# Kernel optimization log

Measured on AMD Instinct MI355X. Metric: run time of the kernel, lower is better.

The kernel has to match this reference:

```python
import jax, jax.numpy as jnp
import numpy as np

COMMITMENT_COST = 0.25
DECAY = 0.99
EPSILON = 1e-05


def setup_inputs() -> dict:
    key = jax.random.key(0)
    k1, k2, k3, k4 = jax.random.split(key, 4)
    S, B, D, K = 256, 64, 512, 4096
    return {
        "inputs": jax.random.normal(k1, (S, B, D), dtype=jnp.float32),
        "embedding_weight": jax.random.normal(k2, (K, D), dtype=jnp.float32),
        "ema_w": jax.random.normal(k3, (K, D), dtype=jnp.float32),
        "ema_cluster_size": jax.random.uniform(k4, (K,), dtype=jnp.float32),
    }


def reference(inputs, embedding_weight, ema_w, ema_cluster_size):
    S, B, D = inputs.shape
    K = embedding_weight.shape[0]
    flat = inputs.reshape(-1, D)  # [N, D], N = S*B

    distances = (
        jnp.sum(flat * flat, axis=1, keepdims=True)
        + jnp.sum(embedding_weight * embedding_weight, axis=1)
        - 2.0 * flat @ embedding_weight.T
    )
    encoding_indices = jnp.argmin(distances, axis=1)  # [N]
    encodings = jax.nn.one_hot(encoding_indices, K, dtype=inputs.dtype)  # [N, K]

    # gather codebook rows (equivalent to encodings @ weight)
    quantized = jnp.take(embedding_weight, encoding_indices, axis=0).reshape(S, B, D)
    encodings_flat = encodings.reshape(S, B, K)

    # EMA codebook update (training-mode buffers; computed with stop_gradient semantics)
    counts = jnp.sum(encodings, axis=0)  # [K]
    new_cluster_size = ema_cluster_size * DECAY + (1.0 - DECAY) * counts
    n = jnp.sum(new_cluster_size)
    new_cluster_size = (new_cluster_size + EPSILON) / (n + K * EPSILON) * n
    dw = jax.ops.segment_sum(flat, encoding_indices, num_segments=K)  # encodings.T @ flat
    new_ema_w = ema_w * DECAY + (1.0 - DECAY) * dw
    new_embedding_weight = new_ema_w / new_cluster_size[:, None]

    # commitment loss (quantized detached)
    e_latent_loss = jnp.mean((jax.lax.stop_gradient(quantized) - inputs) ** 2)
    loss = COMMITMENT_COST * e_latent_loss

    # straight-through estimator
    quantized_st = inputs + jax.lax.stop_gradient(quantized - inputs)

    return (
        loss,
        quantized_st,
        encodings_flat,
        encoding_indices[:, None],
        new_embedding_weight,
        new_cluster_size,
        new_ema_w,
    )
```

## Files before the change

### kernel.cpp

```cpp
#include <hip/hip_runtime.h>
#include <hip/hip_bf16.h>
#include <cstdint>
#include <cstddef>

typedef __attribute__((ext_vector_type(8))) short short8;
typedef __attribute__((ext_vector_type(4))) float f32x4;

#define D_DIM 512
#define K_DIM 4096
#define N_ROWS 16384

#define DECAY_F 0.99f
#define OMD_F 0.01f
#define EPS_F 1e-5f
#define COMMIT_F 0.25f
#define MARGIN_F 0.75f

#define OFF_LOSS 0
#define OFF_QST 1
#define OFF_ENC (1 + 8388608)
#define OFF_IDX (OFF_ENC + 67108864)
#define OFF_NEW_W (OFF_IDX + 16384)
#define OFF_NEW_CS (OFF_NEW_W + 2097152)
#define OFF_NEW_EMA (OFF_NEW_CS + 4096)

#define WS_MINKEY 0
#define WS_COUNTS 131072
#define WS_E2 147456
#define WS_LOSSP 163840
#define WS_RCNT 164096
#define WS_OFFS 164112
#define WS_CURS 180496
#define WS_ROWL 196880
#define WS_ARENA 262416

#define AR_M1K 0
#define AR_M2V 4194304
#define AR_XHI 6291456
#define AR_EHI 23068672
#define AR_RROW 27262976
#define AR_RCUT 27328512
#define AR_NEED 27394048
#define WS_NEED (WS_ARENA + AR_NEED)

#define SCR0 8388612

__device__ __forceinline__ unsigned long long mkkey(float d, int c) {
  unsigned u = __float_as_uint(d);
  u ^= (unsigned)(((int)u) >> 31) | 0x80000000u;
  return ((unsigned long long)u << 32) | (unsigned)c;
}
__device__ __forceinline__ float keyval(unsigned long long k) {
  unsigned u = (unsigned)(k >> 32);
  u = (u & 0x80000000u) ? (u ^ 0x80000000u) : ~u;
  return __uint_as_float(u);
}
__device__ __forceinline__ void merge2(unsigned long long& k1, float& v2,
                                       unsigned long long ko, float v2o) {
  float v1 = keyval(k1), v1o = keyval(ko);
  float vmax = fmaxf(v1, v1o);
  v2 = fminf(fminf(v2, v2o), vmax);
  if (ko < k1) k1 = ko;
}
__device__ __forceinline__ unsigned pk2o(float a, float b) {
  unsigned ua = (__float_as_uint(a) + 0x8000u) & 0xFFFF0000u;
  unsigned ub = (__float_as_uint(b) + 0x8000u) & 0xFFFF0000u;
  return (ua >> 16) | ub;
}
__device__ __forceinline__ void gl_lds16(const void* g, void* l) {
  __builtin_amdgcn_global_load_lds(
      (const __attribute__((address_space(1))) unsigned int*)g,
      (__attribute__((address_space(3))) unsigned int*)l, 16, 0, 0);
}

__global__ void k_e2(const float* __restrict__ E, float* __restrict__ e2,
                     uint4* __restrict__ ehi, int* __restrict__ counts,
                     float* __restrict__ loss_part, int* __restrict__ rcnt) {
  int tid = threadIdx.x;
  int lane = tid & 63;
  int w = tid >> 6;
  int k = blockIdx.x * 4 + w;
  if (tid < 4) counts[blockIdx.x * 4 + tid] = 0;
  if (blockIdx.x == 0 && tid < 64) loss_part[tid] = 0.f;
  if (blockIdx.x == 1 && tid == 0) *rcnt = 0;
  const float4* ev = (const float4*)(E + (size_t)k * D_DIM);
  float4 a = ev[lane * 2], b = ev[lane * 2 + 1];
  uint4 h;
  h.x = pk2o(a.x, a.y);
  h.y = pk2o(a.z, a.w);
  h.z = pk2o(b.x, b.y);
  h.w = pk2o(b.z, b.w);
  ehi[(size_t)k * 64 + lane] = h;
  float s = a.x * a.x + a.y * a.y + a.z * a.z + a.w * a.w +
            b.x * b.x + b.y * b.y + b.z * b.z + b.w * b.w;
#pragma unroll
  for (int off = 32; off > 0; off >>= 1) s += __shfl_down(s, off, 64);
  if (lane == 0) e2[k] = s;
}

__global__ void k_conv(const float* __restrict__ src, uint4* __restrict__ hi) {
  int t = blockIdx.x * 256 + threadIdx.x;
  const float4* s4 = (const float4*)src;
  float4 a = s4[t * 2], b = s4[t * 2 + 1];
  uint4 h;
  h.x = pk2o(a.x, a.y);
  h.y = pk2o(a.z, a.w);
  h.z = pk2o(b.x, b.y);
  h.w = pk2o(b.z, b.w);
  hi[t] = h;
}

__global__ void k_scale_emaw(const float* __restrict__ ema_w, float* __restrict__ out) {
  int i = blockIdx.x * 256 + threadIdx.x;
  out[OFF_NEW_EMA + i] = DECAY_F * ema_w[i];
}

__global__ __launch_bounds__(256, 2) void k_gemm(
    const char* __restrict__ xhi, const char* __restrict__ ehi,
    const float* __restrict__ e2, unsigned long long* __restrict__ m1k,
    float* __restrict__ m2v, float* outp, int doZero) {
  extern __shared__ char smem[];
  const int tid = threadIdx.x;
  const int w = tid >> 6, lane = tid & 63;
  const int wr = w >> 1, wc = w & 1;
  const int l15 = lane & 15, g = lane >> 4;
  const int row0 = blockIdx.x * 128;
  const int col0 = blockIdx.y * 128;

  const char* srcBase = (w < 2) ? xhi : ehi;
  const int srcRow0 = (w < 2) ? (row0 + 64 * w) : (col0 + 64 * (w - 2));
  const int lr = lane >> 3;
  const int lc = lane & 7;
  const char* srcLane = srcBase + (size_t)(srcRow0 + lr) * 1024 + ((lc ^ lr) << 4);
  const int dstOff = w * 8192;

#define STAGE(c, b)                                       \
  {                                                       \
    const char* sp_ = srcLane + (c) * 128;                \
    char* lb_ = smem + (b) * 32768 + dstOff;              \
    _Pragma("unroll") for (int q = 0; q < 8; ++q)         \
        gl_lds16(sp_ + q * 8192, lb_ + q * 1024);         \
  }

  f32x4 acc[4][4];
  const f32x4 z = {0.f, 0.f, 0.f, 0.f};
#pragma unroll
  for (int i = 0; i < 4; ++i)
#pragma unroll
    for (int j = 0; j < 4; ++j) acc[i][j] = z;

  STAGE(0, 0);
  const int s0 = (g ^ (l15 & 7)) << 4;
  const int aRow = (wr * 64 + l15) * 128;
  const int bRow = (wc * 64 + l15) * 128;

  for (int c = 0; c < 8; ++c) {
    __syncthreads();
    if (c < 7) STAGE(c + 1, (c + 1) & 1);
    const char* Ab = smem + (c & 1) * 32768;
    const char* Bb = Ab + 16384;
    short8 a[2][4], b[2][4];
#pragma unroll
    for (int kk = 0; kk < 2; ++kk) {
      const int sw = s0 ^ (kk << 6);
#pragma unroll
      for (int i = 0; i < 4; ++i) {
        a[kk][i] = *(const short8*)(Ab + aRow + i * 2048 + sw);
        b[kk][i] = *(const short8*)(Bb + bRow + i * 2048 + sw);
      }
    }
#pragma unroll
    for (int kk = 0; kk < 2; ++kk)
#pragma unroll
      for (int i = 0; i < 4; ++i)
#pragma unroll
        for (int j = 0; j < 4; ++j)
          acc[i][j] = __builtin_amdgcn_mfma_f32_16x16x32_bf16(a[kk][i], b[kk][j], acc[i][j], 0, 0, 0);
  }
#undef STAGE

  __syncthreads();
  unsigned long long* lk = (unsigned long long*)smem;
  float* lv = (float*)(smem + 2048);
  float e2v[4];
#pragma unroll
  for (int j = 0; j < 4; ++j) e2v[j] = e2[col0 + wc * 64 + j * 16 + l15];

#pragma unroll
  for (int i = 0; i < 4; ++i) {
    int rowl = wr * 64 + i * 16 + (g << 2);
#pragma unroll
    for (int r = 0; r < 4; ++r) {
      unsigned long long k1 = 0;
      float v2 = 3.4e38f;
#pragma unroll
      for (int j = 0; j < 4; ++j) {
        float dv = fmaf(-2.f, acc[i][j][r], e2v[j]);
        unsigned long long kk = mkkey(dv, col0 + wc * 64 + j * 16 + l15);
        if (j == 0) k1 = kk;
        else merge2(k1, v2, kk, 3.4e38f);
      }
#pragma unroll
      for (int m = 1; m <= 8; m <<= 1) {
        unsigned long long ko = __shfl_xor(k1, m, 64);
        float vo = __shfl_xor(v2, m, 64);
        merge2(k1, v2, ko, vo);
      }
      if (l15 == 0) {
        lk[(rowl + r) * 2 + wc] = k1;
        lv[(rowl + r) * 2 + wc] = v2;
      }
    }
  }
  __syncthreads();
  if (tid < 128) {
    unsigned long long k1 = lk[tid * 2];
    float v2 = lv[tid * 2];
    merge2(k1, v2, lk[tid * 2 + 1], lv[tid * 2 + 1]);
    size_t o = (size_t)(row0 + tid) * 32 + blockIdx.y;
    m1k[o] = k1;
    m2v[o] = v2;
  }

  if (doZero) {
    const f32x4 z4 = {0.f, 0.f, 0.f, 0.f};
    float* encm1 = outp + (size_t)OFF_ENC - 1 + (size_t)row0 * K_DIM + col0;
#pragma unroll
    for (int q = 0; q < 16; ++q) {
      int s = tid + 256 * q;
      int r = s >> 5, c4 = s & 31;
      float* p = encm1 + (size_t)r * K_DIM + c4 * 4;
      if (row0 == 0 && col0 == 0 && s == 0) {
        outp[OFF_ENC + 0] = 0.f;
        outp[OFF_ENC + 1] = 0.f;
        outp[OFF_ENC + 2] = 0.f;
      } else {
        __builtin_nontemporal_store(z4, (f32x4*)p);
      }
    }
  }
}

__global__ void k_reduce(const unsigned long long* __restrict__ m1k,
                         const float* __restrict__ m2v,
                         unsigned long long* __restrict__ minkey,
                         int* __restrict__ rcnt, int* __restrict__ rrows,
                         float* __restrict__ rcut) {
  int row = blockIdx.x * 256 + threadIdx.x;
  const unsigned long long* kp = m1k + (size_t)row * 32;
  const float* vp = m2v + (size_t)row * 32;
  unsigned long long k1 = kp[0];
  float v2 = vp[0];
#pragma unroll 4
  for (int t = 1; t < 32; ++t) merge2(k1, v2, kp[t], vp[t]);
  float v1 = keyval(k1);
  if (v2 - v1 < MARGIN_F) {
    minkey[row] = ~0ull;
    int p = atomicAdd(rcnt, 1);
    rrows[p] = row;
    rcut[p] = v1 + MARGIN_F;
  } else {
    minkey[row] = k1;
  }
}

__global__ __launch_bounds__(256) void k_rescue(
    const float* __restrict__ flat, const float* __restrict__ E,
    const float* __restrict__ e2, const int* __restrict__ rcnt,
    const int* __restrict__ rrows, const float* __restrict__ rcut,
    const unsigned long long* __restrict__ m1k,
    unsigned long long* __restrict__ minkey) {
  __shared__ float sx[512];
  __shared__ unsigned long long skey[16];
  const int tid = threadIdx.x;
  const int sl = tid & 15;
  int cnt = *rcnt;
  if (cnt > N_ROWS) cnt = N_ROWS;
  for (int j = (int)blockIdx.x; j < cnt; j += (int)gridDim.x) {
    const int row = rrows[j];
    const float cutoff = rcut[j];
    __syncthreads();
    if (tid < 128) ((float4*)sx)[tid] = ((const float4*)(flat + (size_t)row * 512))[tid];
    __syncthreads();
    unsigned long long best = ~0ull;
    for (int b = 0; b < 32; ++b) {
      if (keyval(m1k[(size_t)row * 32 + b]) >= cutoff) continue;
      const int c0 = b * 128 + (tid >> 4);
#pragma unroll 2
      for (int p = 0; p < 8; ++p) {
        const int c = c0 + p * 16;
        const float4* ev = (const float4*)(E + (size_t)c * 512) + sl * 8;
        const float4* xv = (const float4*)sx + sl * 8;
        float s = 0.f;
#pragma unroll
        for (int q = 0; q < 8; ++q) {
          float4 e4 = ev[q];
          float4 x4 = xv[q];
          s = fmaf(e4.x, x4.x, s);
          s = fmaf(e4.y, x4.y, s);
          s = fmaf(e4.z, x4.z, s);
          s = fmaf(e4.w, x4.w, s);
        }
#pragma unroll
        for (int m = 1; m <= 8; m <<= 1) s += __shfl_xor(s, m, 64);
        if (sl == 0) {
          unsigned long long k = mkkey(fmaf(-2.f, s, e2[c]), c);
          if (k < best) best = k;
        }
      }
    }
    if (sl == 0) skey[tid >> 4] = best;
    __syncthreads();
    if (tid == 0) {
      unsigned long long m = skey[0];
#pragma unroll
      for (int t = 1; t < 16; ++t)
        if (skey[t] < m) m = skey[t];
      atomicMin(&minkey[row], m);
    }
  }
}

__global__ void k_zero(float* __restrict__ out) {
  const f32x4 z = {0.f, 0.f, 0.f, 0.f};
  f32x4* out4 = (f32x4*)(out + 8388612);
#pragma unroll
  for (int t = 0; t < 4; ++t) {
    int i = blockIdx.x * 1024 + t * 256 + threadIdx.x;
    if (i < 16777215) __builtin_nontemporal_store(z, out4 + i);
  }
  if (blockIdx.x == 0 && threadIdx.x == 0) {
    out[8388609] = 0.f;
    out[8388610] = 0.f;
    out[8388611] = 0.f;
    out[75497472] = 0.f;
  }
}

__global__ __launch_bounds__(1024) void k_prefix(const unsigned long long* __restrict__ minkey,
                                                 int* __restrict__ counts,
                                                 int* __restrict__ offs,
                                                 int* __restrict__ cursor) {
  __shared__ int lc[4096];
  __shared__ int wsum[16];
  const int tid = threadIdx.x;
  const int lane = tid & 63, w = tid >> 6;
#pragma unroll
  for (int t = 0; t < 4; ++t) lc[tid * 4 + t] = 0;
  __syncthreads();
#pragma unroll
  for (int t = 0; t < 16; ++t) {
    int c = (int)(unsigned)(minkey[tid + 1024 * t] & 0xffffffffull);
    atomicAdd(&lc[c], 1);
  }
  __syncthreads();
  int v[4];
  int loc = 0;
#pragma unroll
  for (int t = 0; t < 4; ++t) {
    v[t] = lc[tid * 4 + t];
    loc += v[t];
  }
  int scan = loc;
#pragma unroll
  for (int off = 1; off <= 32; off <<= 1) {
    int o = __shfl_up(scan, off, 64);
    if (lane >= off) scan += o;
  }
  if (lane == 63) wsum[w] = scan;
  __syncthreads();
  int base = 0;
  for (int i = 0; i < w; ++i) base += wsum[i];
  int run = base + scan - loc;
#pragma unroll
  for (int t = 0; t < 4; ++t) {
    counts[tid * 4 + t] = v[t];
    offs[tid * 4 + t] = run;
    cursor[tid * 4 + t] = run;
    run += v[t];
  }
}

__global__ void k_scatter(const unsigned long long* __restrict__ minkey,
                          int* __restrict__ cursor, int* __restrict__ rowl) {
  int n = blockIdx.x * 256 + threadIdx.x;
  int c = (int)(unsigned)(minkey[n] & 0xffffffffull);
  int pos = atomicAdd(&cursor[c], 1);
  rowl[pos] = n;
}

__global__ __launch_bounds__(256) void k_qdw(const float* __restrict__ flat,
                                             const float* __restrict__ E,
                                             const float* __restrict__ ema_w,
                                             const int* __restrict__ counts,
                                             const int* __restrict__ offs,
                                             const int* __restrict__ rowl,
                                             float* __restrict__ out,
                                             float* __restrict__ loss_part) {
  const int k = blockIdx.x;
  const int tid = threadIdx.x;
  const int cnt = counts[k];
  const int off = offs[k];
  const int d0 = tid * 2;
  const float ex = E[(size_t)k * D_DIM + d0];
  const float ey = E[(size_t)k * D_DIM + d0 + 1];
  float s0 = 0.f, s1 = 0.f, lsum = 0.f;
  for (int i = 0; i < cnt; ++i) {
    int r = rowl[off + i];
    const float* xr = flat + (size_t)r * D_DIM + d0;
    float xx = xr[0], xy = xr[1];
    size_t qb = (size_t)OFF_QST + (size_t)r * D_DIM + d0;
    out[qb] = xx + (ex - xx);
    out[qb + 1] = xy + (ey - xy);
    float dx = ex - xx, dy = ey - xy;
    lsum += dx * dx + dy * dy;
    s0 += xx;
    s1 += xy;
  }
  float e0 = DECAY_F * ema_w[(size_t)k * D_DIM + d0] + OMD_F * s0;
  float e1 = DECAY_F * ema_w[(size_t)k * D_DIM + d0 + 1] + OMD_F * s1;
  float cs = out[OFF_NEW_CS + k];
  size_t b = (size_t)k * D_DIM + d0;
  out[OFF_NEW_EMA + b] = e0;
  out[OFF_NEW_EMA + b + 1] = e1;
  out[OFF_NEW_W + b] = e0 / cs;
  out[OFF_NEW_W + b + 1] = e1 / cs;
#pragma unroll
  for (int o = 32; o > 0; o >>= 1) lsum += __shfl_down(lsum, o, 64);
  __shared__ float ws4[4];
  if ((tid & 63) == 0) ws4[tid >> 6] = lsum;
  __syncthreads();
  if (tid == 0 && cnt > 0)
    atomicAdd(&loss_part[k & 63], ws4[0] + ws4[1] + ws4[2] + ws4[3]);
}

__global__ void k_quant(const float* __restrict__ flat, const float* __restrict__ E,
                        const unsigned long long* __restrict__ minkey,
                        float* __restrict__ out, float* emaw,
                        float* __restrict__ loss_part) {
  int tid = threadIdx.x;
  int lane = tid & 63;
  int rw = tid >> 6;
  int n = blockIdx.x * 4 + rw;
  int idx = (int)(unsigned)(minkey[n] & 0xffffffffull);
  const float4* xv = (const float4*)(flat + (size_t)n * D_DIM);
  const float4* ev = (const float4*)(E + (size_t)idx * D_DIM);
  float* emarow = emaw + (size_t)idx * D_DIM;
  float s = 0.f;
#pragma unroll
  for (int t = 0; t < 2; ++t) {
    int p = lane + 64 * t;
    float4 x = xv[p];
    float4 e = ev[p];
    size_t qb = (size_t)OFF_QST + (size_t)n * D_DIM + (size_t)p * 4;
    out[qb + 0] = x.x + (e.x - x.x);
    out[qb + 1] = x.y + (e.y - x.y);
    out[qb + 2] = x.z + (e.z - x.z);
    out[qb + 3] = x.w + (e.w - x.w);
    float dx = e.x - x.x, dy = e.y - x.y, dz = e.z - x.z, dw = e.w - x.w;
    s += dx * dx + dy * dy + dz * dz + dw * dw;
    atomicAdd(emarow + p * 4 + 0, OMD_F * x.x);
    atomicAdd(emarow + p * 4 + 1, OMD_F * x.y);
    atomicAdd(emarow + p * 4 + 2, OMD_F * x.z);
    atomicAdd(emarow + p * 4 + 3, OMD_F * x.w);
  }
#pragma unroll
  for (int off = 32; off > 0; off >>= 1) s += __shfl_down(s, off, 64);
  __shared__ float ws4[4];
  if (lane == 0) ws4[rw] = s;
  __syncthreads();
  if (tid == 0) atomicAdd(&loss_part[blockIdx.x & 63], ws4[0] + ws4[1] + ws4[2] + ws4[3]);
}

__global__ void k_decode(const unsigned long long* __restrict__ minkey,
                         int* __restrict__ counts,
                         const float* __restrict__ loss_part,
                         float* __restrict__ out, int withCounts, int withLoss) {
  int n = blockIdx.x * 256 + threadIdx.x;
  int c = (int)(unsigned)(minkey[n] & 0xffffffffull);
  out[OFF_IDX + n] = (float)c;
  if (withCounts) atomicAdd(&counts[c], 1);
  if (n == N_ROWS - 1) out[(size_t)OFF_ENC + (size_t)n * K_DIM + 4095] = 0.f;
  out[(size_t)OFF_ENC + (size_t)n * K_DIM + c] = 1.0f;
  if (withLoss && blockIdx.x == 0 && threadIdx.x < 64) {
    float lv = loss_part[threadIdx.x];
#pragma unroll
    for (int off = 32; off > 0; off >>= 1) lv += __shfl_down(lv, off, 64);
    if (threadIdx.x == 0) out[OFF_LOSS] = COMMIT_F * lv / 8388608.0f;
  }
}

__global__ __launch_bounds__(1024) void k_cs(const float* __restrict__ ema_cs,
                                             const int* __restrict__ counts,
                                             const float* __restrict__ loss_part,
                                             float* __restrict__ out, int withLoss) {
  int tid = threadIdx.x;
  float cs1[4];
  float local = 0.f;
#pragma unroll
  for (int t = 0; t < 4; ++t) {
    int k = tid + 1024 * t;
    cs1[t] = ema_cs[k] * DECAY_F + OMD_F * (float)counts[k];
    local += cs1[t];
  }
  __shared__ float wsum[16];
  float v = local;
#pragma unroll
  for (int off = 32; off > 0; off >>= 1) v += __shfl_down(v, off, 64);
  if ((tid & 63) == 0) wsum[tid >> 6] = v;
  __syncthreads();
  float n_total = 0.f;
#pragma unroll
  for (int t = 0; t < 16; ++t) n_total += wsum[t];
  float scale = n_total / (n_total + (float)K_DIM * EPS_F);
#pragma unroll
  for (int t = 0; t < 4; ++t) {
    int k = tid + 1024 * t;
    out[OFF_NEW_CS + k] = (cs1[t] + EPS_F) * scale;
  }
  if (withLoss && tid < 64) {
    float lv = loss_part[tid];
#pragma unroll
    for (int off = 32; off > 0; off >>= 1) lv += __shfl_down(lv, off, 64);
    if (tid == 0) out[OFF_LOSS] = COMMIT_F * lv / 8388608.0f;
  }
}

__global__ void k_final(float* __restrict__ out) {
  int i = blockIdx.x * 256 + threadIdx.x;
  int k = i >> 9;
  out[OFF_NEW_W + i] = out[OFF_NEW_EMA + i] / out[OFF_NEW_CS + k];
}

extern "C" void kernel_launch(void* const* d_in, const int* in_sizes, int n_in,
                              void* d_out, int out_size, void* d_ws, size_t ws_size,
                              hipStream_t stream) {
  (void)in_sizes; (void)n_in; (void)out_size;
  const float* flat = (const float*)d_in[0];
  const float* E = (const float*)d_in[1];
  const float* ema_w = (const float*)d_in[2];
  const float* ema_cs = (const float*)d_in[3];
  float* out = (float*)d_out;
  char* ws = (char*)d_ws;

  unsigned long long* minkey = (unsigned long long*)(ws + WS_MINKEY);
  int* counts = (int*)(ws + WS_COUNTS);
  float* e2 = (float*)(ws + WS_E2);
  float* loss_part = (float*)(ws + WS_LOSSP);
  int* rcnt = (int*)(ws + WS_RCNT);
  int* offs = (int*)(ws + WS_OFFS);
  int* cursor = (int*)(ws + WS_CURS);
  int* rowl = (int*)(ws + WS_ROWL);

  const bool big = ws_size >= (size_t)WS_NEED;
  char* arena = big ? (ws + WS_ARENA) : (char*)(out + SCR0);
  unsigned long long* m1k = (unsigned long long*)(arena + AR_M1K);
  float* m2v = (float*)(arena + AR_M2V);
  char* xhi = arena + AR_XHI;
  char* ehi = arena + AR_EHI;
  int* rrows = (int*)(arena + AR_RROW);
  float* rcut = (float*)(arena + AR_RCUT);

  k_e2<<<1024, 256, 0, stream>>>(E, e2, (uint4*)ehi, counts, loss_part, rcnt);
  k_conv<<<4096, 256, 0, stream>>>(flat, (uint4*)xhi);
  if (big) {
    k_gemm<<<dim3(128, 32), 256, 65536, stream>>>(xhi, ehi, e2, m1k, m2v, out, 1);
    k_reduce<<<64, 256, 0, stream>>>(m1k, m2v, minkey, rcnt, rrows, rcut);
    k_rescue<<<2048, 256, 0, stream>>>(flat, E, e2, rcnt, rrows, rcut, m1k, minkey);
    k_prefix<<<1, 1024, 0, stream>>>(minkey, counts, offs, cursor);
    k_scatter<<<64, 256, 0, stream>>>(minkey, cursor, rowl);
    k_cs<<<1, 1024, 0, stream>>>(ema_cs, counts, loss_part, out, 0);
    k_qdw<<<4096, 256, 0, stream>>>(flat, E, ema_w, counts, offs, rowl, out, loss_part);
    k_decode<<<64, 256, 0, stream>>>(minkey, counts, loss_part, out, 0, 1);
  } else {
    k_scale_emaw<<<8192, 256, 0, stream>>>(ema_w, out);
    k_gemm<<<dim3(128, 32), 256, 65536, stream>>>(xhi, ehi, e2, m1k, m2v, out, 0);
    k_reduce<<<64, 256, 0, stream>>>(m1k, m2v, minkey, rcnt, rrows, rcut);
    k_rescue<<<2048, 256, 0, stream>>>(flat, E, e2, rcnt, rrows, rcut, m1k, minkey);
    k_zero<<<16384, 256, 0, stream>>>(out);
    k_decode<<<64, 256, 0, stream>>>(minkey, counts, loss_part, out, 1, 0);
    k_quant<<<4096, 256, 0, stream>>>(flat, E, minkey, out, out + OFF_NEW_EMA, loss_part);
    k_cs<<<1, 1024, 0, stream>>>(ema_cs, counts, loss_part, out, 1);
    k_final<<<8192, 256, 0, stream>>>(out);
  }
}
```

Before: 391.2 us.

## Spread one-hot zero-fill across extra blocks in e2, conv, gemm and rescue kernels

```diff
diff --git a/kernel.cpp b/kernel.cpp
--- a/kernel.cpp
+++ b/kernel.cpp
@@ -23,6 +23,18 @@
 #define OFF_NEW_W (OFF_IDX + 16384)
 #define OFF_NEW_CS (OFF_NEW_W + 2097152)
 #define OFF_NEW_EMA (OFF_NEW_CS + 4096)
+
+#define ENC4_CNT 16777215
+#define CHUNK4 8192
+
+#define CB_E2 0
+#define NC_E2 64
+#define CB_CONV 64
+#define NC_CONV 192
+#define CB_GEMM 256
+#define NC_GEMM 1408
+#define CB_RESC 1664
+#define NC_RESC 384
 
 #define WS_MINKEY 0
 #define WS_COUNTS 131072
@@ -73,9 +85,31 @@
       (__attribute__((address_space(3))) unsigned int*)l, 16, 0, 0);
 }
 
+__device__ __forceinline__ void enc_chunk(float* __restrict__ out, int cid) {
+  const f32x4 z = {0.f, 0.f, 0.f, 0.f};
+  f32x4* p = (f32x4*)(out + 8388612);
+  const int base = cid * CHUNK4;
+  const int tid = threadIdx.x;
+#pragma unroll
+  for (int t = 0; t < 32; ++t) {
+    int i = base + t * 256 + tid;
+    if (i < ENC4_CNT) __builtin_nontemporal_store(z, p + i);
+  }
+  if (cid == 0 && tid == 0) {
+    out[8388609] = 0.f;
+    out[8388610] = 0.f;
+    out[8388611] = 0.f;
+  }
+}
+
 __global__ void k_e2(const float* __restrict__ E, float* __restrict__ e2,
                      uint4* __restrict__ ehi, int* __restrict__ counts,
-                     float* __restrict__ loss_part, int* __restrict__ rcnt) {
+                     float* __restrict__ loss_part, int* __restrict__ rcnt,
+                     float* outp) {
+  if (blockIdx.x >= 1024) {
+    enc_chunk(outp, CB_E2 + (int)blockIdx.x - 1024);
+    return;
+  }
   int tid = threadIdx.x;
   int lane = tid & 63;
   int w = tid >> 6;
@@ -98,7 +132,12 @@
   if (lane == 0) e2[k] = s;
 }
 
-__global__ void k_conv(const float* __restrict__ src, uint4* __restrict__ hi) {
+__global__ void k_conv(const float* __restrict__ src, uint4* __restrict__ hi,
+                       float* outp) {
+  if (blockIdx.x >= 4096) {
+    enc_chunk(outp, CB_CONV + (int)blockIdx.x - 4096);
+    return;
+  }
   int t = blockIdx.x * 256 + threadIdx.x;
   const float4* s4 = (const float4*)src;
   float4 a = s4[t * 2], b = s4[t * 2 + 1];
@@ -118,7 +157,11 @@
 __global__ __launch_bounds__(256, 2) void k_gemm(
     const char* __restrict__ xhi, const char* __restrict__ ehi,
     const float* __restrict__ e2, unsigned long long* __restrict__ m1k,
-    float* __restrict__ m2v, float* outp, int doZero) {
+    float* __restrict__ m2v, float* outp) {
+  if (blockIdx.x >= 128) {
+    enc_chunk(outp, CB_GEMM + ((int)blockIdx.x - 128) * 32 + (int)blockIdx.y);
+    return;
+  }
   extern __shared__ char smem[];
   const int tid = threadIdx.x;
   const int w = tid >> 6, lane = tid & 63;
@@ -220,24 +263,6 @@
     size_t o = (size_t)(row0 + tid) * 32 + blockIdx.y;
     m1k[o] = k1;
     m2v[o] = v2;
-  }
-
-  if (doZero) {
-    const f32x4 z4 = {0.f, 0.f, 0.f, 0.f};
-    float* encm1 = outp + (size_t)OFF_ENC - 1 + (size_t)row0 * K_DIM + col0;
-#pragma unroll
-    for (int q = 0; q < 16; ++q) {
-      int s = tid + 256 * q;
-      int r = s >> 5, c4 = s & 31;
-      float* p = encm1 + (size_t)r * K_DIM + c4 * 4;
-      if (row0 == 0 && col0 == 0 && s == 0) {
-        outp[OFF_ENC + 0] = 0.f;
-        outp[OFF_ENC + 1] = 0.f;
-        outp[OFF_ENC + 2] = 0.f;
-      } else {
-        __builtin_nontemporal_store(z4, (f32x4*)p);
-      }
-    }
   }
 }
 
@@ -269,14 +294,18 @@
     const float* __restrict__ e2, const int* __restrict__ rcnt,
     const int* __restrict__ rrows, const float* __restrict__ rcut,
     const unsigned long long* __restrict__ m1k,
-    unsigned long long* __restrict__ minkey) {
+    unsigned long long* __restrict__ minkey, float* outp, int nmain, int cbase) {
+  if ((int)blockIdx.x >= nmain) {
+    enc_chunk(outp, cbase + (int)blockIdx.x - nmain);
+    return;
+  }
   __shared__ float sx[512];
   __shared__ unsigned long long skey[16];
   const int tid = threadIdx.x;
   const int sl = tid & 15;
   int cnt = *rcnt;
   if (cnt > N_ROWS) cnt = N_ROWS;
-  for (int j = (int)blockIdx.x; j < cnt; j += (int)gridDim.x) {
+  for (int j = (int)blockIdx.x; j < cnt; j += nmain) {
     const int row = rrows[j];
     const float cutoff = rcut[j];
     __syncthreads();
@@ -417,6 +446,11 @@
     s0 += xx;
     s1 += xy;
   }
+  for (int i = tid; i < cnt; i += 256) {
+    int r = rowl[off + i];
+    out[OFF_IDX + r] = (float)k;
+    out[(size_t)OFF_ENC + (size_t)r * K_DIM + k] = 1.0f;
+  }
   float e0 = DECAY_F * ema_w[(size_t)k * D_DIM + d0] + OMD_F * s0;
   float e1 = DECAY_F * ema_w[(size_t)k * D_DIM + d0 + 1] + OMD_F * s1;
   float cs = out[OFF_NEW_CS + k];
@@ -432,6 +466,13 @@
   __syncthreads();
   if (tid == 0 && cnt > 0)
     atomicAdd(&loss_part[k & 63], ws4[0] + ws4[1] + ws4[2] + ws4[3]);
+}
+
+__global__ void k_loss(const float* __restrict__ loss_part, float* __restrict__ out) {
+  float lv = loss_part[threadIdx.x];
+#pragma unroll
+  for (int off = 32; off > 0; off >>= 1) lv += __shfl_down(lv, off, 64);
+  if (threadIdx.x == 0) out[OFF_LOSS] = COMMIT_F * lv / 8388608.0f;
 }
 
 __global__ void k_quant(const float* __restrict__ flat, const float* __restrict__ E,
@@ -473,27 +514,19 @@
 }
 
 __global__ void k_decode(const unsigned long long* __restrict__ minkey,
-                         int* __restrict__ counts,
-                         const float* __restrict__ loss_part,
-                         float* __restrict__ out, int withCounts, int withLoss) {
+                         int* __restrict__ counts, float* __restrict__ out) {
   int n = blockIdx.x * 256 + threadIdx.x;
   int c = (int)(unsigned)(minkey[n] & 0xffffffffull);
   out[OFF_IDX + n] = (float)c;
-  if (withCounts) atomicAdd(&counts[c], 1);
-  if (n == N_ROWS - 1) out[(size_t)OFF_ENC + (size_t)n * K_DIM + 4095] = 0.f;
+  atomicAdd(&counts[c], 1);
   out[(size_t)OFF_ENC + (size_t)n * K_DIM + c] = 1.0f;
-  if (withLoss && blockIdx.x == 0 && threadIdx.x < 64) {
-    float lv = loss_part[threadIdx.x];
-#pragma unroll
-    for (int off = 32; off > 0; off >>= 1) lv += __shfl_down(lv, off, 64);
-    if (threadIdx.x == 0) out[OFF_LOSS] = COMMIT_F * lv / 8388608.0f;
-  }
 }
 
 __global__ __launch_bounds__(1024) void k_cs(const float* __restrict__ ema_cs,
                                              const int* __restrict__ counts,
                                              const float* __restrict__ loss_part,
-                                             float* __restrict__ out, int withLoss) {
+                                             float* __restrict__ out, int withLoss,
+                                             int patchTail) {
   int tid = threadIdx.x;
   float cs1[4];
   float local = 0.f;
@@ -518,6 +551,7 @@
     int k = tid + 1024 * t;
     out[OFF_NEW_CS + k] = (cs1[t] + EPS_F) * scale;
   }
+  if (patchTail && tid == 0) out[75497472] = 0.f;
   if (withLoss && tid < 64) {
     float lv = loss_part[tid];
 #pragma unroll
@@ -561,26 +595,32 @@
   int* rrows = (int*)(arena + AR_RROW);
   float* rcut = (float*)(arena + AR_RCUT);
 
-  k_e2<<<1024, 256, 0, stream>>>(E, e2, (uint4*)ehi, counts, loss_part, rcnt);
-  k_conv<<<4096, 256, 0, stream>>>(flat, (uint4*)xhi);
   if (big) {
-    k_gemm<<<dim3(128, 32), 256, 65536, stream>>>(xhi, ehi, e2, m1k, m2v, out, 1);
+    k_e2<<<1024 + NC_E2, 256, 0, stream>>>(E, e2, (uint4*)ehi, counts, loss_part,
+                                           rcnt, out);
+    k_conv<<<4096 + NC_CONV, 256, 0, stream>>>(flat, (uint4*)xhi, out);
+    k_gemm<<<dim3(128 + NC_GEMM / 32, 32), 256, 65536, stream>>>(xhi, ehi, e2, m1k,
+                                                                 m2v, out);
     k_reduce<<<64, 256, 0, stream>>>(m1k, m2v, minkey, rcnt, rrows, rcut);
-    k_rescue<<<2048, 256, 0, stream>>>(flat, E, e2, rcnt, rrows, rcut, m1k, minkey);
+    k_rescue<<<1024 + NC_RESC, 256, 0, stream>>>(flat, E, e2, rcnt, rrows, rcut,
+                                                 m1k, minkey, out, 1024, CB_RESC);
     k_prefix<<<1, 1024, 0, stream>>>(minkey, counts, offs, cursor);
     k_scatter<<<64, 256, 0, stream>>>(minkey, cursor, rowl);
-    k_cs<<<1, 1024, 0, stream>>>(ema_cs, counts, loss_part, out, 0);
+    k_cs<<<1, 1024, 0, stream>>>(ema_cs, counts, loss_part, out, 0, 1);
     k_qdw<<<4096, 256, 0, stream>>>(flat, E, ema_w, counts, offs, rowl, out, loss_part);
-    k_decode<<<64, 256, 0, stream>>>(minkey, counts, loss_part, out, 0, 1);
+    k_loss<<<1, 64, 0, stream>>>(loss_part, out);
   } else {
+    k_e2<<<1024, 256, 0, stream>>>(E, e2, (uint4*)ehi, counts, loss_part, rcnt, out);
+    k_conv<<<4096, 256, 0, stream>>>(flat, (uint4*)xhi, out);
     k_scale_emaw<<<8192, 256, 0, stream>>>(ema_w, out);
-    k_gemm<<<dim3(128, 32), 256, 65536, stream>>>(xhi, ehi, e2, m1k, m2v, out, 0);
+    k_gemm<<<dim3(128, 32), 256, 65536, stream>>>(xhi, ehi, e2, m1k, m2v, out);
     k_reduce<<<64, 256, 0, stream>>>(m1k, m2v, minkey, rcnt, rrows, rcut);
-    k_rescue<<<2048, 256, 0, stream>>>(flat, E, e2, rcnt, rrows, rcut, m1k, minkey);
+    k_rescue<<<2048, 256, 0, stream>>>(flat, E, e2, rcnt, rrows, rcut, m1k, minkey,
+                                       out, 2048, 0);
     k_zero<<<16384, 256, 0, stream>>>(out);
-    k_decode<<<64, 256, 0, stream>>>(minkey, counts, loss_part, out, 1, 0);
+    k_decode<<<64, 256, 0, stream>>>(minkey, counts, out);
     k_quant<<<4096, 256, 0, stream>>>(flat, E, minkey, out, out + OFF_NEW_EMA, loss_part);
-    k_cs<<<1, 1024, 0, stream>>>(ema_cs, counts, loss_part, out, 1);
+    k_cs<<<1, 1024, 0, stream>>>(ema_cs, counts, loss_part, out, 1, 0);
     k_final<<<8192, 256, 0, stream>>>(out);
   }
 }
```

After: 388.7 us. Within noise of the previous version (-0.6%).

## Zero encodings by checking existing contents, fold one-hot writes into qdw

Applied to the files above, without the earlier changes.

```diff
diff --git a/kernel.cpp b/kernel.cpp
--- a/kernel.cpp
+++ b/kernel.cpp
@@ -5,6 +5,7 @@
 
 typedef __attribute__((ext_vector_type(8))) short short8;
 typedef __attribute__((ext_vector_type(4))) float f32x4;
+typedef __attribute__((ext_vector_type(4))) unsigned int u32x4;
 
 #define D_DIM 512
 #define K_DIM 4096
@@ -23,6 +24,9 @@
 #define OFF_NEW_W (OFF_IDX + 16384)
 #define OFF_NEW_CS (OFF_NEW_W + 2097152)
 #define OFF_NEW_EMA (OFF_NEW_CS + 4096)
+
+#define ENC4_CNT 16777215
+#define CHUNK4 8192
 
 #define WS_MINKEY 0
 #define WS_COUNTS 131072
@@ -71,6 +75,34 @@
   __builtin_amdgcn_global_load_lds(
       (const __attribute__((address_space(1))) unsigned int*)g,
       (__attribute__((address_space(3))) unsigned int*)l, 16, 0, 0);
+}
+
+__device__ __forceinline__ void enc_chunk(float* __restrict__ out, int cid) {
+  const f32x4 z = {0.f, 0.f, 0.f, 0.f};
+  const u32x4* p = (const u32x4*)(out + 8388612);
+  const int tid = threadIdx.x;
+  const int base = cid * CHUNK4 + tid;
+#pragma unroll
+  for (int h = 0; h < 2; ++h) {
+    u32x4 v[16];
+#pragma unroll
+    for (int t = 0; t < 16; ++t) {
+      int i = base + (h * 16 + t) * 256;
+      int ii = (i < ENC4_CNT) ? i : 0;
+      v[t] = __builtin_nontemporal_load(p + ii);
+    }
+#pragma unroll
+    for (int t = 0; t < 16; ++t) {
+      int i = base + (h * 16 + t) * 256;
+      if (i < ENC4_CNT && (v[t].x | v[t].y | v[t].z | v[t].w))
+        *(f32x4*)(p + i) = z;
+    }
+  }
+  if (cid == 0 && tid == 0) {
+    if (__float_as_uint(out[8388609])) out[8388609] = 0.f;
+    if (__float_as_uint(out[8388610])) out[8388610] = 0.f;
+    if (__float_as_uint(out[8388611])) out[8388611] = 0.f;
+  }
 }
 
 __global__ void k_e2(const float* __restrict__ E, float* __restrict__ e2,
@@ -118,7 +150,11 @@
 __global__ __launch_bounds__(256, 2) void k_gemm(
     const char* __restrict__ xhi, const char* __restrict__ ehi,
     const float* __restrict__ e2, unsigned long long* __restrict__ m1k,
-    float* __restrict__ m2v, float* outp, int doZero) {
+    float* __restrict__ m2v, float* outp, int withClean) {
+  if (blockIdx.x >= 128) {
+    enc_chunk(outp, ((int)blockIdx.x - 128) * 32 + (int)blockIdx.y);
+    return;
+  }
   extern __shared__ char smem[];
   const int tid = threadIdx.x;
   const int w = tid >> 6, lane = tid & 63;
@@ -126,6 +162,7 @@
   const int l15 = lane & 15, g = lane >> 4;
   const int row0 = blockIdx.x * 128;
   const int col0 = blockIdx.y * 128;
+  (void)withClean;
 
   const char* srcBase = (w < 2) ? xhi : ehi;
   const int srcRow0 = (w < 2) ? (row0 + 64 * w) : (col0 + 64 * (w - 2));
@@ -220,24 +257,6 @@
     size_t o = (size_t)(row0 + tid) * 32 + blockIdx.y;
     m1k[o] = k1;
     m2v[o] = v2;
-  }
-
-  if (doZero) {
-    const f32x4 z4 = {0.f, 0.f, 0.f, 0.f};
-    float* encm1 = outp + (size_t)OFF_ENC - 1 + (size_t)row0 * K_DIM + col0;
-#pragma unroll
-    for (int q = 0; q < 16; ++q) {
-      int s = tid + 256 * q;
-      int r = s >> 5, c4 = s & 31;
-      float* p = encm1 + (size_t)r * K_DIM + c4 * 4;
-      if (row0 == 0 && col0 == 0 && s == 0) {
-        outp[OFF_ENC + 0] = 0.f;
-        outp[OFF_ENC + 1] = 0.f;
-        outp[OFF_ENC + 2] = 0.f;
-      } else {
-        __builtin_nontemporal_store(z4, (f32x4*)p);
-      }
-    }
   }
 }
 
@@ -417,6 +436,11 @@
     s0 += xx;
     s1 += xy;
   }
+  for (int i = tid; i < cnt; i += 256) {
+    int r = rowl[off + i];
+    out[OFF_IDX + r] = (float)k;
+    out[(size_t)OFF_ENC + (size_t)r * K_DIM + k] = 1.0f;
+  }
   float e0 = DECAY_F * ema_w[(size_t)k * D_DIM + d0] + OMD_F * s0;
   float e1 = DECAY_F * ema_w[(size_t)k * D_DIM + d0 + 1] + OMD_F * s1;
   float cs = out[OFF_NEW_CS + k];
@@ -432,6 +456,13 @@
   __syncthreads();
   if (tid == 0 && cnt > 0)
     atomicAdd(&loss_part[k & 63], ws4[0] + ws4[1] + ws4[2] + ws4[3]);
+}
+
+__global__ void k_loss(const float* __restrict__ loss_part, float* __restrict__ out) {
+  float lv = loss_part[threadIdx.x];
+#pragma unroll
+  for (int off = 32; off > 0; off >>= 1) lv += __shfl_down(lv, off, 64);
+  if (threadIdx.x == 0) out[OFF_LOSS] = COMMIT_F * lv / 8388608.0f;
 }
 
 __global__ void k_quant(const float* __restrict__ flat, const float* __restrict__ E,
@@ -473,27 +504,19 @@
 }
 
 __global__ void k_decode(const unsigned long long* __restrict__ minkey,
-                         int* __restrict__ counts,
-                         const float* __restrict__ loss_part,
-                         float* __restrict__ out, int withCounts, int withLoss) {
+                         int* __restrict__ counts, float* __restrict__ out) {
   int n = blockIdx.x * 256 + threadIdx.x;
   int c = (int)(unsigned)(minkey[n] & 0xffffffffull);
   out[OFF_IDX + n] = (float)c;
-  if (withCounts) atomicAdd(&counts[c], 1);
-  if (n == N_ROWS - 1) out[(size_t)OFF_ENC + (size_t)n * K_DIM + 4095] = 0.f;
+  atomicAdd(&counts[c], 1);
   out[(size_t)OFF_ENC + (size_t)n * K_DIM + c] = 1.0f;
-  if (withLoss && blockIdx.x == 0 && threadIdx.x < 64) {
-    float lv = loss_part[threadIdx.x];
-#pragma unroll
-    for (int off = 32; off > 0; off >>= 1) lv += __shfl_down(lv, off, 64);
-    if (threadIdx.x == 0) out[OFF_LOSS] = COMMIT_F * lv / 8388608.0f;
-  }
 }
 
 __global__ __launch_bounds__(1024) void k_cs(const float* __restrict__ ema_cs,
                                              const int* __restrict__ counts,
                                              const float* __restrict__ loss_part,
-                                             float* __restrict__ out, int withLoss) {
+                                             float* __restrict__ out, int withLoss,
+                                             int patchTail) {
   int tid = threadIdx.x;
   float cs1[4];
   float local = 0.f;
@@ -518,6 +541,7 @@
     int k = tid + 1024 * t;
     out[OFF_NEW_CS + k] = (cs1[t] + EPS_F) * scale;
   }
+  if (patchTail && tid == 0 && __float_as_uint(out[75497472])) out[75497472] = 0.f;
   if (withLoss && tid < 64) {
     float lv = loss_part[tid];
 #pragma unroll
@@ -564,23 +588,23 @@
   k_e2<<<1024, 256, 0, stream>>>(E, e2, (uint4*)ehi, counts, loss_part, rcnt);
   k_conv<<<4096, 256, 0, stream>>>(flat, (uint4*)xhi);
   if (big) {
-    k_gemm<<<dim3(128, 32), 256, 65536, stream>>>(xhi, ehi, e2, m1k, m2v, out, 1);
+    k_gemm<<<dim3(192, 32), 256, 65536, stream>>>(xhi, ehi, e2, m1k, m2v, out, 1);
     k_reduce<<<64, 256, 0, stream>>>(m1k, m2v, minkey, rcnt, rrows, rcut);
     k_rescue<<<2048, 256, 0, stream>>>(flat, E, e2, rcnt, rrows, rcut, m1k, minkey);
     k_prefix<<<1, 1024, 0, stream>>>(minkey, counts, offs, cursor);
     k_scatter<<<64, 256, 0, stream>>>(minkey, cursor, rowl);
-    k_cs<<<1, 1024, 0, stream>>>(ema_cs, counts, loss_part, out, 0);
+    k_cs<<<1, 1024, 0, stream>>>(ema_cs, counts, loss_part, out, 0, 1);
     k_qdw<<<4096, 256, 0, stream>>>(flat, E, ema_w, counts, offs, rowl, out, loss_part);
-    k_decode<<<64, 256, 0, stream>>>(minkey, counts, loss_part, out, 0, 1);
+    k_loss<<<1, 64, 0, stream>>>(loss_part, out);
   } else {
     k_scale_emaw<<<8192, 256, 0, stream>>>(ema_w, out);
     k_gemm<<<dim3(128, 32), 256, 65536, stream>>>(xhi, ehi, e2, m1k, m2v, out, 0);
     k_reduce<<<64, 256, 0, stream>>>(m1k, m2v, minkey, rcnt, rrows, rcut);
     k_rescue<<<2048, 256, 0, stream>>>(flat, E, e2, rcnt, rrows, rcut, m1k, minkey);
     k_zero<<<16384, 256, 0, stream>>>(out);
-    k_decode<<<64, 256, 0, stream>>>(minkey, counts, loss_part, out, 1, 0);
+    k_decode<<<64, 256, 0, stream>>>(minkey, counts, out);
     k_quant<<<4096, 256, 0, stream>>>(flat, E, minkey, out, out + OFF_NEW_EMA, loss_part);
-    k_cs<<<1, 1024, 0, stream>>>(ema_cs, counts, loss_part, out, 1);
+    k_cs<<<1, 1024, 0, stream>>>(ema_cs, counts, loss_part, out, 1, 0);
     k_final<<<8192, 256, 0, stream>>>(out);
   }
 }
```

After: 389.2 us. About the same (-0.5%).
